# Performance work log

Measured on AMD Instinct MI355X. Metric: run time of the kernel, lower is better.

Reference implementation:

```python
import jax, jax.numpy as jnp
import numpy as np

B, S, DIM, H, FFN = 2, 2048, 1024, 16, 4096
HD = DIM // H
THETA = 10000.0
EPS = 1e-5


def setup_inputs() -> dict:
    key = jax.random.key(0)
    ks = jax.random.split(key, 12)
    s = 0.02
    return {
        "x": jax.random.normal(ks[0], (B, S, DIM), jnp.float32),
        "padding_mask": jnp.zeros((B, S), jnp.bool_),
        "qkv_w": jax.random.normal(ks[1], (DIM, 3 * DIM), jnp.float32) * s,
        "qkv_b": jnp.zeros((3 * DIM,), jnp.float32),
        "out_w": jax.random.normal(ks[2], (DIM, DIM), jnp.float32) * s,
        "out_b": jnp.zeros((DIM,), jnp.float32),
        "ln1_g": jnp.ones((DIM,), jnp.float32),
        "ln1_b": jnp.zeros((DIM,), jnp.float32),
        "ln2_g": jnp.ones((DIM,), jnp.float32),
        "ln2_b": jnp.zeros((DIM,), jnp.float32),
        "w1": jax.random.normal(ks[3], (DIM, FFN), jnp.float32) * s,
        "b1": jnp.zeros((FFN,), jnp.float32),
        "w2": jax.random.normal(ks[4], (FFN, DIM), jnp.float32) * s,
        "b2": jnp.zeros((DIM,), jnp.float32),
    }


def _layer_norm(x, g, b):
    mu = jnp.mean(x, axis=-1, keepdims=True)
    var = jnp.mean(jnp.square(x - mu), axis=-1, keepdims=True)
    return (x - mu) * jax.lax.rsqrt(var + EPS) * g + b


def _rotate_half(x):
    x1, x2 = jnp.split(x, 2, axis=-1)
    return jnp.concatenate([-x2, x1], axis=-1)


def reference(x, padding_mask, qkv_w, qkv_b, out_w, out_b,
              ln1_g, ln1_b, ln2_g, ln2_b, w1, b1, w2, b2):
    b, s, _ = x.shape
    residual = x
    h = _layer_norm(x, ln1_g, ln1_b)
    qkv = h @ qkv_w + qkv_b  # [b, s, 3*dim]
    q, k, v = jnp.split(qkv, 3, axis=-1)
    # [b, heads, s, head_dim]
    q = q.reshape(b, s, H, HD).transpose(0, 2, 1, 3)
    k = k.reshape(b, s, H, HD).transpose(0, 2, 1, 3)
    v = v.reshape(b, s, H, HD).transpose(0, 2, 1, 3)

    # rotary embeddings
    pos = jnp.arange(s, dtype=jnp.float32)
    inv_freq = 1.0 / (THETA ** (jnp.arange(0, HD, 2, dtype=jnp.float32) / HD))
    freqs = pos[:, None] * inv_freq[None, :]          # [s, hd/2]
    emb = jnp.concatenate([freqs, freqs], axis=-1)    # [s, hd]
    sin = jnp.sin(emb)[None, None, :, :]
    cos = jnp.cos(emb)[None, None, :, :]
    q = q * cos + _rotate_half(q) * sin
    k = k * cos + _rotate_half(k) * sin

    scale = HD ** (-0.5)
    scores = jnp.einsum('bhqd,bhkd->bhqk', q, k) * scale
    neg = jnp.finfo(scores.dtype).min
    scores = jnp.where(padding_mask[:, None, None, :], neg, scores)
    probs = jax.nn.softmax(scores, axis=-1)
    ctx = jnp.einsum('bhqk,bhkd->bhqd', probs, v)
    ctx = ctx.transpose(0, 2, 1, 3).reshape(b, s, DIM)
    x = residual + (ctx @ out_w + out_b)

    residual = x
    h = _layer_norm(x, ln2_g, ln2_b)
    h = jax.nn.gelu(h @ w1 + b1, approximate=False) @ w2 + b2
    return residual + h
```

## Files before the change

### kernel.cpp

```cpp
#include <hip/hip_runtime.h>
#include <hip/hip_bf16.h>
#include <math.h>

typedef __hip_bfloat16 bf16;
typedef __attribute__((ext_vector_type(8))) short short8;
typedef __attribute__((ext_vector_type(4))) float floatx4;

constexpr int BB   = 2;
constexpr int SS   = 2048;
constexpr int DIMc = 1024;
constexpr int Hc   = 16;
constexpr int HDc  = 64;
constexpr int FFNc = 4096;
constexpr int TOK  = BB * SS;
constexpr float EPSc = 1e-5f;

typedef __attribute__((address_space(1))) void gvoid;
typedef __attribute__((address_space(3))) void lvoid;
__device__ __forceinline__ void lds16(const void* g, void* l) {
    __builtin_amdgcn_global_load_lds((gvoid*)g, (lvoid*)l, 16, 0, 0);
}

__device__ __forceinline__ float fexp2(float x) { return __builtin_amdgcn_exp2f(x); }

__global__ __launch_bounds__(256) void ln_kernel(const float* __restrict__ x,
                                                 const float* __restrict__ g,
                                                 const float* __restrict__ b,
                                                 bf16* __restrict__ out) {
    int t = blockIdx.x;
    int tid = threadIdx.x;
    const float4* xr = (const float4*)(x + (size_t)t * DIMc);
    float4 v = xr[tid];
    float s  = v.x + v.y + v.z + v.w;
    float sq = v.x*v.x + v.y*v.y + v.z*v.z + v.w*v.w;
    for (int off = 1; off < 64; off <<= 1) {
        s  += __shfl_xor(s,  off, 64);
        sq += __shfl_xor(sq, off, 64);
    }
    __shared__ float ss[4], ssq[4];
    int wave = tid >> 6;
    if ((tid & 63) == 0) { ss[wave] = s; ssq[wave] = sq; }
    __syncthreads();
    s  = ss[0] + ss[1] + ss[2] + ss[3];
    sq = ssq[0] + ssq[1] + ssq[2] + ssq[3];
    float mu  = s * (1.0f / DIMc);
    float var = sq * (1.0f / DIMc) - mu * mu;
    float inv = rsqrtf(var + EPSc);
    float4 gg = ((const float4*)g)[tid];
    float4 bb = ((const float4*)b)[tid];
    size_t base = (size_t)t * DIMc + tid * 4;
    out[base + 0] = __float2bfloat16((v.x - mu) * inv * gg.x + bb.x);
    out[base + 1] = __float2bfloat16((v.y - mu) * inv * gg.y + bb.y);
    out[base + 2] = __float2bfloat16((v.z - mu) * inv * gg.z + bb.z);
    out[base + 3] = __float2bfloat16((v.w - mu) * inv * gg.w + bb.w);
}

__global__ __launch_bounds__(256) void reduce_ln_kernel(const float* __restrict__ P,
                                                        const float* __restrict__ x,
                                                        const float* __restrict__ bias,
                                                        const float* __restrict__ g,
                                                        const float* __restrict__ b,
                                                        float* __restrict__ out,
                                                        bf16* __restrict__ hout) {
    int t = blockIdx.x;
    int tid = threadIdx.x;
    size_t off = (size_t)t * DIMc / 4 + tid;
    float4 v  = ((const float4*)x)[off];
    float4 p0 = ((const float4*)P)[off];
    float4 p1 = ((const float4*)P)[off + (size_t)TOK * DIMc / 4];
    float4 bv = ((const float4*)bias)[tid];
    v.x += p0.x + p1.x + bv.x;
    v.y += p0.y + p1.y + bv.y;
    v.z += p0.z + p1.z + bv.z;
    v.w += p0.w + p1.w + bv.w;
    ((float4*)out)[off] = v;

    float s  = v.x + v.y + v.z + v.w;
    float sq = v.x*v.x + v.y*v.y + v.z*v.z + v.w*v.w;
    for (int o = 1; o < 64; o <<= 1) {
        s  += __shfl_xor(s,  o, 64);
        sq += __shfl_xor(sq, o, 64);
    }
    __shared__ float ss[4], ssq[4];
    int wave = tid >> 6;
    if ((tid & 63) == 0) { ss[wave] = s; ssq[wave] = sq; }
    __syncthreads();
    s  = ss[0] + ss[1] + ss[2] + ss[3];
    sq = ssq[0] + ssq[1] + ssq[2] + ssq[3];
    float mu  = s * (1.0f / DIMc);
    float var = sq * (1.0f / DIMc) - mu * mu;
    float inv = rsqrtf(var + EPSc);
    float4 gg = ((const float4*)g)[tid];
    float4 bb = ((const float4*)b)[tid];
    size_t base = (size_t)t * DIMc + tid * 4;
    hout[base + 0] = __float2bfloat16((v.x - mu) * inv * gg.x + bb.x);
    hout[base + 1] = __float2bfloat16((v.y - mu) * inv * gg.y + bb.y);
    hout[base + 2] = __float2bfloat16((v.z - mu) * inv * gg.z + bb.z);
    hout[base + 3] = __float2bfloat16((v.w - mu) * inv * gg.w + bb.w);
}

__global__ __launch_bounds__(256) void reduce_add_kernel(const float* __restrict__ P,
                                                         const float* __restrict__ bias,
                                                         float* __restrict__ out) {
    size_t f = (size_t)blockIdx.x * 256 + threadIdx.x;
    float4 v  = ((float4*)out)[f];
    float4 p0 = ((const float4*)P)[f];
    float4 p1 = ((const float4*)P)[f + (size_t)TOK * DIMc / 4];
    float4 bv = ((const float4*)bias)[f & (DIMc / 4 - 1)];
    v.x += p0.x + p1.x + bv.x;
    v.y += p0.y + p1.y + bv.y;
    v.z += p0.z + p1.z + bv.z;
    v.w += p0.w + p1.w + bv.w;
    ((float4*)out)[f] = v;
}

__global__ __launch_bounds__(256) void transpose_bf16(const float* __restrict__ in,
                                                      bf16* __restrict__ out,
                                                      int K, int N) {
    __shared__ float t[32][33];
    int k0 = blockIdx.y * 32, n0 = blockIdx.x * 32;
    int x = threadIdx.x & 31;
    int y = threadIdx.x >> 5;
#pragma unroll
    for (int i = 0; i < 4; ++i) {
        int k = y + i * 8;
        t[k][x] = in[(size_t)(k0 + k) * N + n0 + x];
    }
    __syncthreads();
#pragma unroll
    for (int i = 0; i < 4; ++i) {
        int n = y + i * 8;
        out[(size_t)(n0 + n) * K + k0 + x] = __float2bfloat16(t[x][n]);
    }
}

template <int ACT, bool ADD_RES, bool OUT_BF16>
__global__ __launch_bounds__(256) void gemm_bt(const bf16* __restrict__ A,
                                               const bf16* __restrict__ Bt,
                                               const float* __restrict__ bias,
                                               const float* __restrict__ res,
                                               void* __restrict__ Cout,
                                               int M, int N, int K) {
    constexpr int BM = 128, BN = 128, BK = 32;
    __shared__ bf16 As[BM * BK];
    __shared__ bf16 Bs[BN * BK];
    const int tid = threadIdx.x;
    const int wave = tid >> 6, lane = tid & 63;
    const int lane15 = lane & 15, lgrp = lane >> 4;
    const int wm = (wave >> 1) * 64, wn = (wave & 1) * 64;
    const int row0 = blockIdx.y * BM, col0 = blockIdx.x * BN;

    floatx4 acc[4][4] = {};

    const int sr = tid >> 2;
    const int sc = (tid & 3) * 8;
    const bf16* ga = A  + (size_t)(row0 + sr) * K + sc;
    const bf16* gb = Bt + (size_t)(col0 + sr) * K + sc;
    bf16* la = As + wave * 512;
    bf16* lb = Bs + wave * 512;

    for (int k0 = 0; k0 < K; k0 += BK) {
        __syncthreads();
        lds16(ga + k0,                  la);
        lds16(ga + k0 + (size_t)64 * K, la + 2048);
        lds16(gb + k0,                  lb);
        lds16(gb + k0 + (size_t)64 * K, lb + 2048);
        __syncthreads();
        short8 af[4], bfr[4];
#pragma unroll
        for (int i = 0; i < 4; ++i)
            af[i] = *(const short8*)(As + (wm + i * 16 + lane15) * BK + lgrp * 8);
#pragma unroll
        for (int j = 0; j < 4; ++j)
            bfr[j] = *(const short8*)(Bs + (wn + j * 16 + lane15) * BK + lgrp * 8);
#pragma unroll
        for (int i = 0; i < 4; ++i)
#pragma unroll
            for (int j = 0; j < 4; ++j)
                acc[i][j] = __builtin_amdgcn_mfma_f32_16x16x32_bf16(af[i], bfr[j], acc[i][j], 0, 0, 0);
    }

#pragma unroll
    for (int i = 0; i < 4; ++i) {
#pragma unroll
        for (int j = 0; j < 4; ++j) {
            int col = col0 + wn + j * 16 + lane15;
            float bv = bias[col];
#pragma unroll
            for (int r = 0; r < 4; ++r) {
                int row = row0 + wm + i * 16 + lgrp * 4 + r;
                float v = acc[i][j][r] + bv;
                if (ACT == 1) v = 0.5f * v * (1.0f + erff(v * 0.70710678118654752f));
                if (ADD_RES) v += res[(size_t)row * N + col];
                if (OUT_BF16) ((bf16*)Cout)[(size_t)row * N + col] = __float2bfloat16(v);
                else          ((float*)Cout)[(size_t)row * N + col] = v;
            }
        }
    }
}

__global__ __launch_bounds__(256) void gemm_bt_splitk(const bf16* __restrict__ A,
                                                      const bf16* __restrict__ Bt,
                                                      float* __restrict__ P,
                                                      int M, int N, int K, int KCH) {
    constexpr int BM = 128, BN = 128, BK = 32;
    __shared__ bf16 As[BM * BK];
    __shared__ bf16 Bs[BN * BK];
    const int tid = threadIdx.x;
    const int wave = tid >> 6, lane = tid & 63;
    const int lane15 = lane & 15, lgrp = lane >> 4;
    const int wm = (wave >> 1) * 64, wn = (wave & 1) * 64;
    const int row0 = blockIdx.y * BM, col0 = blockIdx.x * BN;
    const int kbase = blockIdx.z * KCH;
    float* Cp = P + (size_t)blockIdx.z * M * N;

    floatx4 acc[4][4] = {};

    const int sr = tid >> 2;
    const int sc = (tid & 3) * 8;
    const bf16* ga = A  + (size_t)(row0 + sr) * K + sc;
    const bf16* gb = Bt + (size_t)(col0 + sr) * K + sc;
    bf16* la = As + wave * 512;
    bf16* lb = Bs + wave * 512;

    for (int k0 = kbase; k0 < kbase + KCH; k0 += BK) {
        __syncthreads();
        lds16(ga + k0,                  la);
        lds16(ga + k0 + (size_t)64 * K, la + 2048);
        lds16(gb + k0,                  lb);
        lds16(gb + k0 + (size_t)64 * K, lb + 2048);
        __syncthreads();
        short8 af[4], bfr[4];
#pragma unroll
        for (int i = 0; i < 4; ++i)
            af[i] = *(const short8*)(As + (wm + i * 16 + lane15) * BK + lgrp * 8);
#pragma unroll
        for (int j = 0; j < 4; ++j)
            bfr[j] = *(const short8*)(Bs + (wn + j * 16 + lane15) * BK + lgrp * 8);
#pragma unroll
        for (int i = 0; i < 4; ++i)
#pragma unroll
            for (int j = 0; j < 4; ++j)
                acc[i][j] = __builtin_amdgcn_mfma_f32_16x16x32_bf16(af[i], bfr[j], acc[i][j], 0, 0, 0);
    }

#pragma unroll
    for (int i = 0; i < 4; ++i)
#pragma unroll
        for (int j = 0; j < 4; ++j) {
            int col = col0 + wn + j * 16 + lane15;
#pragma unroll
            for (int r = 0; r < 4; ++r) {
                int row = row0 + wm + i * 16 + lgrp * 4 + r;
                Cp[(size_t)row * N + col] = acc[i][j][r];
            }
        }
}

__global__ __launch_bounds__(256) void rope_kernel(bf16* __restrict__ qkv) {
    int t = blockIdx.x;
    int pos = t % SS;
    int tid = threadIdx.x;
    const float ln_theta = 9.210340371976184f;
    for (int idx = tid; idx < 1024; idx += 256) {
        int which = idx >> 9;
        int p = idx & 511;
        int head = p >> 5, d = p & 31;
        float inv_freq = __expf(-((float)(2 * d) / (float)HDc) * ln_theta);
        float ang = (float)pos * inv_freq;
        float sn, cs;
        __sincosf(ang, &sn, &cs);
        size_t base = (size_t)t * (3 * DIMc) + (size_t)which * DIMc + head * HDc + d;
        float x1 = __bfloat162float(qkv[base]);
        float x2 = __bfloat162float(qkv[base + 32]);
        qkv[base]      = __float2bfloat16(x1 * cs - x2 * sn);
        qkv[base + 32] = __float2bfloat16(x2 * cs + x1 * sn);
    }
}

__global__ __launch_bounds__(256) void attn_mfma(const bf16* __restrict__ qkv,
                                                 const unsigned char* __restrict__ mask,
                                                 bf16* __restrict__ ctx) {
    __shared__ short Klds[2][64][32];
    __shared__ short Vt[64][72];
    __shared__ short Ps[4][32][72];
    __shared__ float mkf[64];

    const int b = blockIdx.z, h = blockIdx.y, q0 = blockIdx.x * 128;
    const int tid = threadIdx.x;
    const int wave = tid >> 6, lane = tid & 63;
    const int lane15 = lane & 15, lgrp = lane >> 4;
    const short* qs = (const short*)qkv;

    short* qstage = &Ps[wave][0][0];
#pragma unroll
    for (int i = 0; i < 4; ++i) {
        int idx = i * 64 + lane;
        int g = idx & 3, row = (idx >> 2) & 15, s = (idx >> 6) & 1, mi = idx >> 7;
        const short* gq = qs + (size_t)(b * SS + q0 + wave * 32 + mi * 16 + row) * 3072
                             + h * 64 + s * 32 + g * 8;
        lds16(gq, qstage + idx * 8);
    }
    __syncthreads();
    short8 aQ[2][2];
#pragma unroll
    for (int mi = 0; mi < 2; ++mi)
#pragma unroll
        for (int s = 0; s < 2; ++s)
            aQ[mi][s] = *(const short8*)(qstage + ((mi * 2 + s) * 16 + lane15) * 32 + lgrp * 8);

    const short8 bOnes = (short8)(short)0x3F80;
    floatx4 O[2][4] = {};
    floatx4 Lacc[2] = {};
    const float cscale = 0.18033688011112042f;

    for (int k0 = 0; k0 < SS; k0 += 64) {
        __syncthreads();
#pragma unroll
        for (int i = 0; i < 2; ++i) {
            int idx = wave * 128 + i * 64 + lane;
            int g = idx & 3, row = (idx >> 2) & 63, s = idx >> 8;
            const short* gk = qs + (size_t)(b * SS + k0 + row) * 3072 + 1024
                                 + h * 64 + s * 32 + g * 8;
            lds16(gk, &Klds[0][0][0] + idx * 8);
        }
#pragma unroll
        for (int c = 0; c < 2; ++c) {
            int idx = c * 256 + tid;
            int dgrp = idx >> 6, kk = idx & 63;
            const short8 vv = *(const short8*)(qs + (size_t)(b * SS + k0 + kk) * 3072
                                               + 2048 + h * 64 + dgrp * 8);
#pragma unroll
            for (int j = 0; j < 8; ++j) Vt[dgrp * 8 + j][kk] = vv[j];
        }
        if (tid < 16) {
            const unsigned char* mp = mask + b * SS + k0 + tid * 4;
#pragma unroll
            for (int j = 0; j < 4; ++j) mkf[tid * 4 + j] = mp[j] ? -1e30f : 0.0f;
        }
        __syncthreads();

        short8 bK[4][2];
#pragma unroll
        for (int j = 0; j < 4; ++j)
#pragma unroll
            for (int s = 0; s < 2; ++s)
                bK[j][s] = *(const short8*)&Klds[s][j * 16 + lane15][lgrp * 8];
        floatx4 Sf[2][4] = {};
#pragma unroll
        for (int mi = 0; mi < 2; ++mi)
#pragma unroll
            for (int j = 0; j < 4; ++j)
#pragma unroll
                for (int s = 0; s < 2; ++s)
                    Sf[mi][j] = __builtin_amdgcn_mfma_f32_16x16x32_bf16(aQ[mi][s], bK[j][s], Sf[mi][j], 0, 0, 0);

        float mkv[4];
#pragma unroll
        for (int j = 0; j < 4; ++j) mkv[j] = mkf[j * 16 + lane15];

#pragma unroll
        for (int mi = 0; mi < 2; ++mi)
#pragma unroll
            for (int r = 0; r < 4; ++r)
#pragma unroll
                for (int j = 0; j < 4; ++j) {
                    float p = fexp2(Sf[mi][j][r] * cscale + mkv[j]);
                    bf16 t = __float2bfloat16(p);
                    Ps[wave][mi * 16 + lgrp * 4 + r][lane15 + 16 * j] = *(short*)&t;
                }

        short8 aP[2][2], bV[4][2];
#pragma unroll
        for (int mi = 0; mi < 2; ++mi)
#pragma unroll
            for (int s = 0; s < 2; ++s)
                aP[mi][s] = *(const short8*)&Ps[wave][mi * 16 + lane15][s * 32 + lgrp * 8];
#pragma unroll
        for (int jd = 0; jd < 4; ++jd)
#pragma unroll
            for (int s = 0; s < 2; ++s)
                bV[jd][s] = *(const short8*)&Vt[jd * 16 + lane15][s * 32 + lgrp * 8];
#pragma unroll
        for (int mi = 0; mi < 2; ++mi) {
#pragma unroll
            for (int jd = 0; jd < 4; ++jd)
#pragma unroll
                for (int s = 0; s < 2; ++s)
                    O[mi][jd] = __builtin_amdgcn_mfma_f32_16x16x32_bf16(aP[mi][s], bV[jd][s], O[mi][jd], 0, 0, 0);
#pragma unroll
            for (int s = 0; s < 2; ++s)
                Lacc[mi] = __builtin_amdgcn_mfma_f32_16x16x32_bf16(aP[mi][s], bOnes, Lacc[mi], 0, 0, 0);
        }
    }

#pragma unroll
    for (int mi = 0; mi < 2; ++mi)
#pragma unroll
        for (int r = 0; r < 4; ++r) {
            float inv = 1.0f / Lacc[mi][r];
            size_t rowoff = (size_t)(b * SS + q0 + wave * 32 + mi * 16 + lgrp * 4 + r) * DIMc
                            + h * 64 + lane15;
#pragma unroll
            for (int jd = 0; jd < 4; ++jd)
                ctx[rowoff + jd * 16] = __float2bfloat16(O[mi][jd][r] * inv);
        }
}

extern "C" void kernel_launch(void* const* d_in, const int* in_sizes, int n_in,
                              void* d_out, int out_size, void* d_ws, size_t ws_size,
                              hipStream_t stream) {
    const float* x      = (const float*)d_in[0];
    const unsigned char* pmask = (const unsigned char*)d_in[1];
    const float* qkv_w  = (const float*)d_in[2];
    const float* qkv_b  = (const float*)d_in[3];
    const float* out_w  = (const float*)d_in[4];
    const float* out_b  = (const float*)d_in[5];
    const float* ln1_g  = (const float*)d_in[6];
    const float* ln1_b  = (const float*)d_in[7];
    const float* ln2_g  = (const float*)d_in[8];
    const float* ln2_b  = (const float*)d_in[9];
    const float* w1     = (const float*)d_in[10];
    const float* b1     = (const float*)d_in[11];
    const float* w2     = (const float*)d_in[12];
    const float* b2     = (const float*)d_in[13];
    float* out = (float*)d_out;

    char* ws = (char*)d_ws;
    bf16* wqkv_t = (bf16*)ws;                      ws += (size_t)3072 * 1024 * 2;
    bf16* wout_t = (bf16*)ws;                      ws += (size_t)1024 * 1024 * 2;
    bf16* w1_t   = (bf16*)ws;                      ws += (size_t)4096 * 1024 * 2;
    bf16* w2_t   = (bf16*)ws;                      ws += (size_t)1024 * 4096 * 2;
    bf16* h_bf   = (bf16*)ws;                      ws += (size_t)TOK * DIMc * 2;
    bf16* qkv_bf = (bf16*)ws;                      ws += (size_t)TOK * 3 * DIMc * 2;
    bf16* ctx_bf = (bf16*)ws;                      ws += (size_t)TOK * DIMc * 2;
    float* partial = (float*)ws;                   ws += (size_t)2 * TOK * DIMc * 4;
    bf16* ffn1_bf = qkv_bf;

    transpose_bf16<<<dim3(3072 / 32, 1024 / 32), 256, 0, stream>>>(qkv_w, wqkv_t, 1024, 3072);
    transpose_bf16<<<dim3(1024 / 32, 1024 / 32), 256, 0, stream>>>(out_w, wout_t, 1024, 1024);
    transpose_bf16<<<dim3(4096 / 32, 1024 / 32), 256, 0, stream>>>(w1,    w1_t,   1024, 4096);
    transpose_bf16<<<dim3(1024 / 32, 4096 / 32), 256, 0, stream>>>(w2,    w2_t,   4096, 1024);

    ln_kernel<<<TOK, 256, 0, stream>>>(x, ln1_g, ln1_b, h_bf);
    gemm_bt<0, false, true><<<dim3(3072 / 128, TOK / 128), 256, 0, stream>>>(
        h_bf, wqkv_t, qkv_b, nullptr, qkv_bf, TOK, 3 * DIMc, DIMc);
    rope_kernel<<<TOK, 256, 0, stream>>>(qkv_bf);
    attn_mfma<<<dim3(SS / 128, Hc, BB), 256, 0, stream>>>(qkv_bf, pmask, ctx_bf);

    gemm_bt_splitk<<<dim3(1024 / 128, TOK / 128, 2), 256, 0, stream>>>(
        ctx_bf, wout_t, partial, TOK, DIMc, DIMc, 512);
    reduce_ln_kernel<<<TOK, 256, 0, stream>>>(partial, x, out_b, ln2_g, ln2_b, out, h_bf);

    gemm_bt<1, false, true><<<dim3(4096 / 128, TOK / 128), 256, 0, stream>>>(
        h_bf, w1_t, b1, nullptr, ffn1_bf, TOK, FFNc, DIMc);
    gemm_bt_splitk<<<dim3(1024 / 128, TOK / 128, 2), 256, 0, stream>>>(
        ffn1_bf, w2_t, partial, TOK, DIMc, FFNc, 2048);
    reduce_add_kernel<<<TOK * DIMc / 4 / 256, 256, 0, stream>>>(partial, b2, out);
}
```

Before: 430.2 us.

## Fuse RoPE into QKV GEMM, split attention over keys, pre-transpose V, deepen GEMM K-step

RoPE is now applied in the QKV GEMM epilogue, which removes the separate rope pass over the qkv buffer. V is transposed once into a separate buffer so attention can stream it into LDS with direct global-to-LDS loads instead of scattering it per tile. Attention is split across two key halves to double the grid, with a combine kernel that merges the unnormalized outputs and row sums. The GEMMs also process a 64-wide K step per barrier pair, halving synchronizations. The cost is extra fp32 partial traffic for the combine and an added transpose launch.

```diff
diff --git a/kernel.cpp b/kernel.cpp
--- a/kernel.cpp
+++ b/kernel.cpp
@@ -20,7 +20,6 @@
 __device__ __forceinline__ void lds16(const void* g, void* l) {
     __builtin_amdgcn_global_load_lds((gvoid*)g, (lvoid*)l, 16, 0, 0);
 }
-
 __device__ __forceinline__ float fexp2(float x) { return __builtin_amdgcn_exp2f(x); }
 
 __global__ __launch_bounds__(256) void ln_kernel(const float* __restrict__ x,
@@ -29,8 +28,7 @@
                                                  bf16* __restrict__ out) {
     int t = blockIdx.x;
     int tid = threadIdx.x;
-    const float4* xr = (const float4*)(x + (size_t)t * DIMc);
-    float4 v = xr[tid];
+    float4 v = ((const float4*)(x + (size_t)t * DIMc))[tid];
     float s  = v.x + v.y + v.z + v.w;
     float sq = v.x*v.x + v.y*v.y + v.z*v.z + v.w*v.w;
     for (int off = 1; off < 64; off <<= 1) {
@@ -134,66 +132,113 @@
     }
 }
 
-template <int ACT, bool ADD_RES, bool OUT_BF16>
+__global__ __launch_bounds__(256) void transpose_v(const bf16* __restrict__ qkv,
+                                                   bf16* __restrict__ vT) {
+    __shared__ short t[64][72];
+    const int s0 = blockIdx.x * 64, h = blockIdx.y, b = blockIdx.z;
+    const int tid = threadIdx.x;
+    const short* qs = (const short*)qkv;
+#pragma unroll
+    for (int it = 0; it < 2; ++it) {
+        int idx = it * 256 + tid;
+        int r = idx >> 3, c = (idx & 7) * 8;
+        *(short8*)&t[r][c] = *(const short8*)(qs + (size_t)(b * SS + s0 + r) * 3072
+                                              + 2048 + h * 64 + c);
+    }
+    __syncthreads();
+#pragma unroll
+    for (int it = 0; it < 2; ++it) {
+        int idx = it * 256 + tid;
+        int d = idx >> 3, cs = (idx & 7) * 8;
+        short8 v;
+#pragma unroll
+        for (int j = 0; j < 8; ++j) v[j] = t[cs + j][d];
+        *(short8*)((short*)vT + ((size_t)(b * Hc + h) * 64 + d) * SS + s0 + cs) = v;
+    }
+}
+
+template <int ACT, bool ROPE>
 __global__ __launch_bounds__(256) void gemm_bt(const bf16* __restrict__ A,
                                                const bf16* __restrict__ Bt,
                                                const float* __restrict__ bias,
-                                               const float* __restrict__ res,
-                                               void* __restrict__ Cout,
+                                               bf16* __restrict__ Cout,
                                                int M, int N, int K) {
-    constexpr int BM = 128, BN = 128, BK = 32;
-    __shared__ bf16 As[BM * BK];
-    __shared__ bf16 Bs[BN * BK];
+    constexpr int BK = 64;
+    __shared__ bf16 As[2][128 * 32];
+    __shared__ bf16 Bs[2][128 * 32];
     const int tid = threadIdx.x;
     const int wave = tid >> 6, lane = tid & 63;
     const int lane15 = lane & 15, lgrp = lane >> 4;
     const int wm = (wave >> 1) * 64, wn = (wave & 1) * 64;
-    const int row0 = blockIdx.y * BM, col0 = blockIdx.x * BN;
+    const int row0 = blockIdx.y * 128, col0 = blockIdx.x * 128;
 
     floatx4 acc[4][4] = {};
 
-    const int sr = tid >> 2;
-    const int sc = (tid & 3) * 8;
-    const bf16* ga = A  + (size_t)(row0 + sr) * K + sc;
-    const bf16* gb = Bt + (size_t)(col0 + sr) * K + sc;
-    bf16* la = As + wave * 512;
-    bf16* lb = Bs + wave * 512;
+    const int srow = wave * 16 + (lane >> 2);
+    const int scol = (lane & 3) * 8;
+    const bf16* ga = A  + (size_t)(row0 + srow) * K + scol;
+    const bf16* gb = Bt + (size_t)(col0 + srow) * K + scol;
 
     for (int k0 = 0; k0 < K; k0 += BK) {
         __syncthreads();
-        lds16(ga + k0,                  la);
-        lds16(ga + k0 + (size_t)64 * K, la + 2048);
-        lds16(gb + k0,                  lb);
-        lds16(gb + k0 + (size_t)64 * K, lb + 2048);
+#pragma unroll
+        for (int p = 0; p < 4; ++p) {
+            const size_t go = (size_t)((p & 1) * 64) * K + k0 + (p >> 1) * 32;
+            lds16(ga + go, &As[p >> 1][(p & 1) * 2048 + wave * 512]);
+            lds16(gb + go, &Bs[p >> 1][(p & 1) * 2048 + wave * 512]);
+        }
         __syncthreads();
-        short8 af[4], bfr[4];
-#pragma unroll
-        for (int i = 0; i < 4; ++i)
-            af[i] = *(const short8*)(As + (wm + i * 16 + lane15) * BK + lgrp * 8);
-#pragma unroll
-        for (int j = 0; j < 4; ++j)
-            bfr[j] = *(const short8*)(Bs + (wn + j * 16 + lane15) * BK + lgrp * 8);
-#pragma unroll
-        for (int i = 0; i < 4; ++i)
+#pragma unroll
+        for (int s = 0; s < 2; ++s) {
+            short8 af[4], bfr[4];
+#pragma unroll
+            for (int i = 0; i < 4; ++i)
+                af[i] = *(const short8*)(&As[s][(wm + i * 16 + lane15) * 32 + lgrp * 8]);
 #pragma unroll
             for (int j = 0; j < 4; ++j)
-                acc[i][j] = __builtin_amdgcn_mfma_f32_16x16x32_bf16(af[i], bfr[j], acc[i][j], 0, 0, 0);
-    }
+                bfr[j] = *(const short8*)(&Bs[s][(wn + j * 16 + lane15) * 32 + lgrp * 8]);
+#pragma unroll
+            for (int i = 0; i < 4; ++i)
+#pragma unroll
+                for (int j = 0; j < 4; ++j)
+                    acc[i][j] = __builtin_amdgcn_mfma_f32_16x16x32_bf16(af[i], bfr[j], acc[i][j], 0, 0, 0);
+        }
+    }
+
+    const bool doRope = ROPE && (col0 < 2048);
+    float invf0 = 0.f, invf1 = 0.f;
+    if (ROPE) {
+        invf0 = fexp2(-0.4152410118609203f * (float)lane15);
+        invf1 = fexp2(-0.4152410118609203f * (float)(16 + lane15));
+    }
+    float bv[4];
+#pragma unroll
+    for (int j = 0; j < 4; ++j) bv[j] = bias[col0 + wn + j * 16 + lane15];
 
 #pragma unroll
     for (int i = 0; i < 4; ++i) {
 #pragma unroll
-        for (int j = 0; j < 4; ++j) {
-            int col = col0 + wn + j * 16 + lane15;
-            float bv = bias[col];
-#pragma unroll
-            for (int r = 0; r < 4; ++r) {
-                int row = row0 + wm + i * 16 + lgrp * 4 + r;
-                float v = acc[i][j][r] + bv;
-                if (ACT == 1) v = 0.5f * v * (1.0f + erff(v * 0.70710678118654752f));
-                if (ADD_RES) v += res[(size_t)row * N + col];
-                if (OUT_BF16) ((bf16*)Cout)[(size_t)row * N + col] = __float2bfloat16(v);
-                else          ((float*)Cout)[(size_t)row * N + col] = v;
+        for (int r = 0; r < 4; ++r) {
+            int row = row0 + wm + i * 16 + lgrp * 4 + r;
+            float v[4];
+#pragma unroll
+            for (int j = 0; j < 4; ++j) v[j] = acc[i][j][r] + bv[j];
+            if (doRope) {
+                float pos = (float)(row & (SS - 1));
+                float s0, c0, s1, c1;
+                __sincosf(pos * invf0, &s0, &c0);
+                __sincosf(pos * invf1, &s1, &c1);
+                float t0 = v[0] * c0 - v[2] * s0;
+                float t1 = v[1] * c1 - v[3] * s1;
+                float t2 = v[2] * c0 + v[0] * s0;
+                float t3 = v[3] * c1 + v[1] * s1;
+                v[0] = t0; v[1] = t1; v[2] = t2; v[3] = t3;
+            }
+#pragma unroll
+            for (int j = 0; j < 4; ++j) {
+                float o = v[j];
+                if (ACT == 1) o = 0.5f * o * (1.0f + erff(o * 0.70710678118654752f));
+                Cout[(size_t)row * N + col0 + wn + j * 16 + lane15] = __float2bfloat16(o);
             }
         }
     }
@@ -203,45 +248,48 @@
                                                       const bf16* __restrict__ Bt,
                                                       float* __restrict__ P,
                                                       int M, int N, int K, int KCH) {
-    constexpr int BM = 128, BN = 128, BK = 32;
-    __shared__ bf16 As[BM * BK];
-    __shared__ bf16 Bs[BN * BK];
+    constexpr int BK = 64;
+    __shared__ bf16 As[2][128 * 32];
+    __shared__ bf16 Bs[2][128 * 32];
     const int tid = threadIdx.x;
     const int wave = tid >> 6, lane = tid & 63;
     const int lane15 = lane & 15, lgrp = lane >> 4;
     const int wm = (wave >> 1) * 64, wn = (wave & 1) * 64;
-    const int row0 = blockIdx.y * BM, col0 = blockIdx.x * BN;
+    const int row0 = blockIdx.y * 128, col0 = blockIdx.x * 128;
     const int kbase = blockIdx.z * KCH;
     float* Cp = P + (size_t)blockIdx.z * M * N;
 
     floatx4 acc[4][4] = {};
 
-    const int sr = tid >> 2;
-    const int sc = (tid & 3) * 8;
-    const bf16* ga = A  + (size_t)(row0 + sr) * K + sc;
-    const bf16* gb = Bt + (size_t)(col0 + sr) * K + sc;
-    bf16* la = As + wave * 512;
-    bf16* lb = Bs + wave * 512;
+    const int srow = wave * 16 + (lane >> 2);
+    const int scol = (lane & 3) * 8;
+    const bf16* ga = A  + (size_t)(row0 + srow) * K + scol;
+    const bf16* gb = Bt + (size_t)(col0 + srow) * K + scol;
 
     for (int k0 = kbase; k0 < kbase + KCH; k0 += BK) {
         __syncthreads();
-        lds16(ga + k0,                  la);
-        lds16(ga + k0 + (size_t)64 * K, la + 2048);
-        lds16(gb + k0,                  lb);
-        lds16(gb + k0 + (size_t)64 * K, lb + 2048);
+#pragma unroll
+        for (int p = 0; p < 4; ++p) {
+            const size_t go = (size_t)((p & 1) * 64) * K + k0 + (p >> 1) * 32;
+            lds16(ga + go, &As[p >> 1][(p & 1) * 2048 + wave * 512]);
+            lds16(gb + go, &Bs[p >> 1][(p & 1) * 2048 + wave * 512]);
+        }
         __syncthreads();
-        short8 af[4], bfr[4];
-#pragma unroll
-        for (int i = 0; i < 4; ++i)
-            af[i] = *(const short8*)(As + (wm + i * 16 + lane15) * BK + lgrp * 8);
-#pragma unroll
-        for (int j = 0; j < 4; ++j)
-            bfr[j] = *(const short8*)(Bs + (wn + j * 16 + lane15) * BK + lgrp * 8);
-#pragma unroll
-        for (int i = 0; i < 4; ++i)
+#pragma unroll
+        for (int s = 0; s < 2; ++s) {
+            short8 af[4], bfr[4];
+#pragma unroll
+            for (int i = 0; i < 4; ++i)
+                af[i] = *(const short8*)(&As[s][(wm + i * 16 + lane15) * 32 + lgrp * 8]);
 #pragma unroll
             for (int j = 0; j < 4; ++j)
-                acc[i][j] = __builtin_amdgcn_mfma_f32_16x16x32_bf16(af[i], bfr[j], acc[i][j], 0, 0, 0);
+                bfr[j] = *(const short8*)(&Bs[s][(wn + j * 16 + lane15) * 32 + lgrp * 8]);
+#pragma unroll
+            for (int i = 0; i < 4; ++i)
+#pragma unroll
+                for (int j = 0; j < 4; ++j)
+                    acc[i][j] = __builtin_amdgcn_mfma_f32_16x16x32_bf16(af[i], bfr[j], acc[i][j], 0, 0, 0);
+        }
     }
 
 #pragma unroll
@@ -257,40 +305,24 @@
         }
 }
 
-__global__ __launch_bounds__(256) void rope_kernel(bf16* __restrict__ qkv) {
-    int t = blockIdx.x;
-    int pos = t % SS;
-    int tid = threadIdx.x;
-    const float ln_theta = 9.210340371976184f;
-    for (int idx = tid; idx < 1024; idx += 256) {
-        int which = idx >> 9;
-        int p = idx & 511;
-        int head = p >> 5, d = p & 31;
-        float inv_freq = __expf(-((float)(2 * d) / (float)HDc) * ln_theta);
-        float ang = (float)pos * inv_freq;
-        float sn, cs;
-        __sincosf(ang, &sn, &cs);
-        size_t base = (size_t)t * (3 * DIMc) + (size_t)which * DIMc + head * HDc + d;
-        float x1 = __bfloat162float(qkv[base]);
-        float x2 = __bfloat162float(qkv[base + 32]);
-        qkv[base]      = __float2bfloat16(x1 * cs - x2 * sn);
-        qkv[base + 32] = __float2bfloat16(x2 * cs + x1 * sn);
-    }
-}
-
 __global__ __launch_bounds__(256) void attn_mfma(const bf16* __restrict__ qkv,
+                                                 const bf16* __restrict__ vT,
                                                  const unsigned char* __restrict__ mask,
-                                                 bf16* __restrict__ ctx) {
+                                                 float* __restrict__ Op,
+                                                 float* __restrict__ Lp) {
     __shared__ short Klds[2][64][32];
-    __shared__ short Vt[64][72];
+    __shared__ short Vlds[2][64][32];
     __shared__ short Ps[4][32][72];
     __shared__ float mkf[64];
 
-    const int b = blockIdx.z, h = blockIdx.y, q0 = blockIdx.x * 128;
+    const int h = blockIdx.y;
+    const int b = blockIdx.z >> 1, kc = blockIdx.z & 1;
+    const int q0 = blockIdx.x * 128;
     const int tid = threadIdx.x;
     const int wave = tid >> 6, lane = tid & 63;
     const int lane15 = lane & 15, lgrp = lane >> 4;
     const short* qs = (const short*)qkv;
+    const short* vs = (const short*)vT + (size_t)(b * Hc + h) * 64 * SS;
 
     short* qstage = &Ps[wave][0][0];
 #pragma unroll
@@ -314,7 +346,8 @@
     floatx4 Lacc[2] = {};
     const float cscale = 0.18033688011112042f;
 
-    for (int k0 = 0; k0 < SS; k0 += 64) {
+    for (int t = 0; t < 16; ++t) {
+        const int k0 = kc * 1024 + t * 64;
         __syncthreads();
 #pragma unroll
         for (int i = 0; i < 2; ++i) {
@@ -325,13 +358,11 @@
             lds16(gk, &Klds[0][0][0] + idx * 8);
         }
 #pragma unroll
-        for (int c = 0; c < 2; ++c) {
-            int idx = c * 256 + tid;
-            int dgrp = idx >> 6, kk = idx & 63;
-            const short8 vv = *(const short8*)(qs + (size_t)(b * SS + k0 + kk) * 3072
-                                               + 2048 + h * 64 + dgrp * 8);
-#pragma unroll
-            for (int j = 0; j < 8; ++j) Vt[dgrp * 8 + j][kk] = vv[j];
+        for (int i = 0; i < 2; ++i) {
+            int idx = wave * 128 + i * 64 + lane;
+            int g = idx & 3, drow = (idx >> 2) & 63, s = idx >> 8;
+            const short* gv = vs + (size_t)drow * SS + k0 + s * 32 + g * 8;
+            lds16(gv, &Vlds[0][0][0] + idx * 8);
         }
         if (tid < 16) {
             const unsigned char* mp = mask + b * SS + k0 + tid * 4;
@@ -366,8 +397,8 @@
 #pragma unroll
                 for (int j = 0; j < 4; ++j) {
                     float p = fexp2(Sf[mi][j][r] * cscale + mkv[j]);
-                    bf16 t = __float2bfloat16(p);
-                    Ps[wave][mi * 16 + lgrp * 4 + r][lane15 + 16 * j] = *(short*)&t;
+                    bf16 tt = __float2bfloat16(p);
+                    Ps[wave][mi * 16 + lgrp * 4 + r][lane15 + 16 * j] = *(short*)&tt;
                 }
 
         short8 aP[2][2], bV[4][2];
@@ -380,7 +411,7 @@
         for (int jd = 0; jd < 4; ++jd)
 #pragma unroll
             for (int s = 0; s < 2; ++s)
-                bV[jd][s] = *(const short8*)&Vt[jd * 16 + lane15][s * 32 + lgrp * 8];
+                bV[jd][s] = *(const short8*)&Vlds[s][jd * 16 + lane15][lgrp * 8];
 #pragma unroll
         for (int mi = 0; mi < 2; ++mi) {
 #pragma unroll
@@ -394,17 +425,36 @@
         }
     }
 
+    float* myOp = Op + (size_t)kc * TOK * DIMc;
 #pragma unroll
     for (int mi = 0; mi < 2; ++mi)
 #pragma unroll
         for (int r = 0; r < 4; ++r) {
-            float inv = 1.0f / Lacc[mi][r];
-            size_t rowoff = (size_t)(b * SS + q0 + wave * 32 + mi * 16 + lgrp * 4 + r) * DIMc
-                            + h * 64 + lane15;
+            int q = q0 + wave * 32 + mi * 16 + lgrp * 4 + r;
+            size_t rowoff = (size_t)(b * SS + q) * DIMc + h * 64 + lane15;
 #pragma unroll
             for (int jd = 0; jd < 4; ++jd)
-                ctx[rowoff + jd * 16] = __float2bfloat16(O[mi][jd][r] * inv);
-        }
+                myOp[rowoff + jd * 16] = O[mi][jd][r];
+            if (lane15 == 0)
+                Lp[((size_t)kc * TOK + b * SS + q) * Hc + h] = Lacc[mi][r];
+        }
+}
+
+__global__ __launch_bounds__(256) void attn_combine(const float* __restrict__ Op,
+                                                    const float* __restrict__ Lp,
+                                                    bf16* __restrict__ ctx) {
+    int t = blockIdx.x;
+    int tid = threadIdx.x;
+    int h = tid >> 4;
+    size_t f = (size_t)t * (DIMc / 4) + tid;
+    float4 p0 = ((const float4*)Op)[f];
+    float4 p1 = ((const float4*)Op)[f + (size_t)TOK * DIMc / 4];
+    float inv = 1.0f / (Lp[(size_t)t * Hc + h] + Lp[((size_t)TOK + t) * Hc + h]);
+    size_t base = (size_t)t * DIMc + tid * 4;
+    ctx[base + 0] = __float2bfloat16((p0.x + p1.x) * inv);
+    ctx[base + 1] = __float2bfloat16((p0.y + p1.y) * inv);
+    ctx[base + 2] = __float2bfloat16((p0.z + p1.z) * inv);
+    ctx[base + 3] = __float2bfloat16((p0.w + p1.w) * inv);
 }
 
 extern "C" void kernel_launch(void* const* d_in, const int* in_sizes, int n_in,
@@ -435,7 +485,9 @@
     bf16* qkv_bf = (bf16*)ws;                      ws += (size_t)TOK * 3 * DIMc * 2;
     bf16* ctx_bf = (bf16*)ws;                      ws += (size_t)TOK * DIMc * 2;
     float* partial = (float*)ws;                   ws += (size_t)2 * TOK * DIMc * 4;
+    float* Lp      = (float*)ws;                   ws += (size_t)2 * TOK * Hc * 4;
     bf16* ffn1_bf = qkv_bf;
+    bf16* vT      = h_bf;
 
     transpose_bf16<<<dim3(3072 / 32, 1024 / 32), 256, 0, stream>>>(qkv_w, wqkv_t, 1024, 3072);
     transpose_bf16<<<dim3(1024 / 32, 1024 / 32), 256, 0, stream>>>(out_w, wout_t, 1024, 1024);
@@ -443,17 +495,18 @@
     transpose_bf16<<<dim3(1024 / 32, 4096 / 32), 256, 0, stream>>>(w2,    w2_t,   4096, 1024);
 
     ln_kernel<<<TOK, 256, 0, stream>>>(x, ln1_g, ln1_b, h_bf);
-    gemm_bt<0, false, true><<<dim3(3072 / 128, TOK / 128), 256, 0, stream>>>(
-        h_bf, wqkv_t, qkv_b, nullptr, qkv_bf, TOK, 3 * DIMc, DIMc);
-    rope_kernel<<<TOK, 256, 0, stream>>>(qkv_bf);
-    attn_mfma<<<dim3(SS / 128, Hc, BB), 256, 0, stream>>>(qkv_bf, pmask, ctx_bf);
+    gemm_bt<0, true><<<dim3(3072 / 128, TOK / 128), 256, 0, stream>>>(
+        h_bf, wqkv_t, qkv_b, qkv_bf, TOK, 3 * DIMc, DIMc);
+    transpose_v<<<dim3(SS / 64, Hc, BB), 256, 0, stream>>>(qkv_bf, vT);
+    attn_mfma<<<dim3(SS / 128, Hc, BB * 2), 256, 0, stream>>>(qkv_bf, vT, pmask, partial, Lp);
+    attn_combine<<<TOK, 256, 0, stream>>>(partial, Lp, ctx_bf);
 
     gemm_bt_splitk<<<dim3(1024 / 128, TOK / 128, 2), 256, 0, stream>>>(
         ctx_bf, wout_t, partial, TOK, DIMc, DIMc, 512);
     reduce_ln_kernel<<<TOK, 256, 0, stream>>>(partial, x, out_b, ln2_g, ln2_b, out, h_bf);
 
-    gemm_bt<1, false, true><<<dim3(4096 / 128, TOK / 128), 256, 0, stream>>>(
-        h_bf, w1_t, b1, nullptr, ffn1_bf, TOK, FFNc, DIMc);
+    gemm_bt<1, false><<<dim3(4096 / 128, TOK / 128), 256, 0, stream>>>(
+        h_bf, w1_t, b1, ffn1_bf, TOK, FFNc, DIMc);
     gemm_bt_splitk<<<dim3(1024 / 128, TOK / 128, 2), 256, 0, stream>>>(
         ffn1_bf, w2_t, partial, TOK, DIMc, FFNc, 2048);
     reduce_add_kernel<<<TOK * DIMc / 4 / 256, 256, 0, stream>>>(partial, b2, out);
```

After: 406.2 us. 5.6% less time.
